# Kernel optimization log

Hardware: AMD Instinct MI355X
Metric: run time of the kernel (lower is better)

The kernel has to match this reference:

```python
import jax, jax.numpy as jnp
import numpy as np

B, S, D, H = 4, 2048, 768, 12
DEPTH = D // H


def setup_inputs() -> dict:
    key = jax.random.key(0)
    ks = jax.random.split(key, 8)
    scale = 1.0 / np.sqrt(D)
    inp = {
        "q": jax.random.normal(ks[0], (B, S, D), jnp.float32),
        "k": jax.random.normal(ks[1], (B, S, D), jnp.float32),
        "v": jax.random.normal(ks[2], (B, S, D), jnp.float32),
        # additive mask: 1.0 at disallowed (future) positions, causal
        "mask": jnp.triu(jnp.ones((S, S), jnp.float32), k=1)[None, None, :, :],
        "wq": jax.random.normal(ks[3], (D, D), jnp.float32) * scale,
        "wk": jax.random.normal(ks[4], (D, D), jnp.float32) * scale,
        "wv": jax.random.normal(ks[5], (D, D), jnp.float32) * scale,
        "w_dense": jax.random.normal(ks[6], (D, D), jnp.float32) * scale,
        "b_dense": jnp.zeros((D,), jnp.float32),
    }
    return inp


def _split_heads(x):
    b, s, _ = x.shape
    return x.reshape(b, s, H, DEPTH).transpose(0, 2, 1, 3)  # [B,H,S,depth]


def reference(q, k, v, mask, wq, wk, wv, w_dense, b_dense):
    qh = _split_heads(q @ wq.T)
    kh = _split_heads(k @ wk.T)
    vh = _split_heads(v @ wv.T)
    scale = jnp.sqrt(jnp.float32(DEPTH))
    logits = jnp.einsum("bhqd,bhkd->bhqk", qh, kh) / scale  # [B,H,S,S]
    logits = logits + mask * -1e9
    attn = jax.nn.softmax(logits, axis=-1)
    out = jnp.einsum("bhqk,bhkd->bhqd", attn, vh)
    out = out.transpose(0, 2, 1, 3).reshape(q.shape[0], -1, D)
    return out @ w_dense.T + b_dense
```

## Files before the change

kernel.cpp:

```cpp
#include <hip/hip_runtime.h>

typedef __attribute__((ext_vector_type(8))) short short8;
typedef __attribute__((ext_vector_type(4))) float f32x4;
typedef __attribute__((ext_vector_type(4))) unsigned int uint4v;

static __device__ __forceinline__ unsigned pack2(float x, float y) {
  unsigned ux = __float_as_uint(x) + 0x8000u;
  unsigned uy = __float_as_uint(y) + 0x8000u;
  return __builtin_amdgcn_perm(uy, ux, 0x07060302u);
}
static __device__ __forceinline__ unsigned packt(float x, float y) {
  return __builtin_amdgcn_perm(__float_as_uint(y), __float_as_uint(x), 0x07060302u);
}

#define GLDS(g, l)                                                                     \
  __builtin_amdgcn_global_load_lds((const __attribute__((address_space(1))) void*)(g), \
                                   (__attribute__((address_space(3))) void*)(l), 16, 0, 0)

__global__ __launch_bounds__(256) void cvt_all(const float* __restrict__ q,
                                               const float* __restrict__ k,
                                               const float* __restrict__ v,
                                               const float* __restrict__ w0,
                                               const float* __restrict__ w1,
                                               const float* __restrict__ w2,
                                               const float* __restrict__ w3,
                                               unsigned short* __restrict__ oq,
                                               unsigned short* __restrict__ ok,
                                               unsigned short* __restrict__ ov,
                                               unsigned short* __restrict__ o0,
                                               unsigned short* __restrict__ o1,
                                               unsigned short* __restrict__ o2,
                                               unsigned short* __restrict__ o3) {
  const int bx = blockIdx.x;
  const float* s;
  unsigned short* d;
  long p;
  if (bx < 9216) {
    int seg = bx / 3072;
    s = seg == 0 ? q : seg == 1 ? k : v;
    d = seg == 0 ? oq : seg == 1 ? ok : ov;
    p = (long)(bx - seg * 3072) * 256 + threadIdx.x;
  } else {
    int t = bx - 9216;
    int seg = t / 288;
    s = seg == 0 ? w0 : seg == 1 ? w1 : seg == 2 ? w2 : w3;
    d = seg == 0 ? o0 : seg == 1 ? o1 : seg == 2 ? o2 : o3;
    p = (long)(t - seg * 288) * 256 + threadIdx.x;
  }
  float4 v0 = ((const float4*)s)[2 * p];
  float4 v1 = ((const float4*)s)[2 * p + 1];
  uint4v o;
  o.x = pack2(v0.x, v0.y);
  o.y = pack2(v0.z, v0.w);
  o.z = pack2(v1.x, v1.y);
  o.w = pack2(v1.z, v1.w);
  *(uint4v*)(d + 8 * p) = o;
}

template <int MODE>
static __device__ __forceinline__ void proj_body(const unsigned short* __restrict__ A,
                                                 const unsigned short* __restrict__ W,
                                                 unsigned short* __restrict__ O, int m0,
                                                 int n0, unsigned short* buf,
                                                 float scale) {
  constexpr int K = 768;
  const int tid = threadIdx.x, lane = tid & 63, wave = tid >> 6;
  const int ln = lane & 15, quad = lane >> 4;
  const int wm = (wave & 1) << 6, wn = (wave >> 1) << 6;

  const int o0 = tid << 4, o1 = 4096 + (tid << 4);
  const int cxp = (((tid & 3) ^ ((tid >> 3) & 3)) << 3);
  const unsigned short* gA0 = A + (long)(m0 + (o0 >> 6)) * K + cxp;
  const unsigned short* gA1 = A + (long)(m0 + (o1 >> 6)) * K + cxp;
  const unsigned short* gW0 = W + (long)(n0 + (o0 >> 6)) * K + cxp;
  const unsigned short* gW1 = W + (long)(n0 + (o1 >> 6)) * K + cxp;

  GLDS(gA0, buf + (o0 >> 1));
  GLDS(gA1, buf + (o1 >> 1));
  GLDS(gW0, buf + 8192 + (o0 >> 1));
  GLDS(gW1, buf + 8192 + (o1 >> 1));

  const int qsw = (quad * 8) ^ (((ln >> 1) & 3) << 3);

  f32x4 acc[4][4] = {};
  for (int t = 0; t < 24; t++) {
    const int cur = t & 1, nxt = cur ^ 1;
    const int k1 = (t + 1) << 5;
    __syncthreads();
    if (t < 23) {
      GLDS(gA0 + k1, buf + nxt * 4096 + (o0 >> 1));
      GLDS(gA1 + k1, buf + nxt * 4096 + (o1 >> 1));
      GLDS(gW0 + k1, buf + 8192 + nxt * 4096 + (o0 >> 1));
      GLDS(gW1 + k1, buf + 8192 + nxt * 4096 + (o1 >> 1));
    }
    const unsigned short* As = buf + cur * 4096;
    const unsigned short* Bs = buf + 8192 + cur * 4096;
    short8 af[4], bfr[4];
#pragma unroll
    for (int mi = 0; mi < 4; mi++)
      af[mi] = *(const short8*)(As + (wm + mi * 16 + ln) * 32 + qsw);
#pragma unroll
    for (int ni = 0; ni < 4; ni++)
      bfr[ni] = *(const short8*)(Bs + (wn + ni * 16 + ln) * 32 + qsw);
#pragma unroll
    for (int mi = 0; mi < 4; mi++)
#pragma unroll
      for (int ni = 0; ni < 4; ni++)
        acc[mi][ni] = (MODE == 0)
                          ? __builtin_amdgcn_mfma_f32_16x16x32_bf16(bfr[ni], af[mi],
                                                                    acc[mi][ni], 0, 0, 0)
                          : __builtin_amdgcn_mfma_f32_16x16x32_bf16(af[mi], bfr[ni],
                                                                    acc[mi][ni], 0, 0, 0);
  }

  unsigned short* Ts = buf;
  __syncthreads();
  if (MODE == 0) {
#pragma unroll
    for (int mi = 0; mi < 4; mi++)
#pragma unroll
      for (int ni = 0; ni < 4; ni++) {
        f32x4 v = acc[mi][ni];
        int s = wm + mi * 16 + ln;
        int n = wn + ni * 16 + quad * 4;
        uint2 w2;
        w2.x = pack2(v[0] * scale, v[1] * scale);
        w2.y = pack2(v[2] * scale, v[3] * scale);
        *(uint2*)(Ts + s * 136 + n) = w2;
      }
    __syncthreads();
    const int part = tid & 7, sg0 = tid >> 3;
#pragma unroll
    for (int p = 0; p < 8; p++) {
      int seg = sg0 + p * 32;
      int hh = seg >> 7, s = seg & 127;
      short8 val = *(const short8*)(Ts + s * 136 + hh * 64 + part * 8);
      int gs = m0 + s;
      int bb = gs >> 11, srow = gs & 2047;
      int head = (n0 >> 6) + hh;
      *(short8*)(O + (((long)(bb * 12 + head) * 2048 + srow) << 6) + part * 8) = val;
    }
  } else {
#pragma unroll
    for (int mi = 0; mi < 4; mi++)
#pragma unroll
      for (int ni = 0; ni < 4; ni++) {
        f32x4 v = acc[mi][ni];
        int d = wn + ni * 16 + ln;
        int s = wm + mi * 16 + quad * 4;
        uint2 w2;
        w2.x = pack2(v[0], v[1]);
        w2.y = pack2(v[2], v[3]);
        *(uint2*)(Ts + d * 136 + s) = w2;
      }
    __syncthreads();
    const int part = tid & 15, r0 = tid >> 4;
    const int bb = m0 >> 11, sbase = m0 & 2047;
#pragma unroll
    for (int p = 0; p < 8; p++) {
      int d = r0 + p * 16;
      short8 val = *(const short8*)(Ts + d * 136 + part * 8);
      int head = (n0 >> 6) + (d >> 6);
      int dl = d & 63;
      *(short8*)(O + ((long)(bb * 12 + head) * 64 + dl) * 2048 + sbase + part * 8) = val;
    }
  }
}

__global__ __launch_bounds__(256) void proj_all(
    const unsigned short* __restrict__ qb, const unsigned short* __restrict__ kb,
    const unsigned short* __restrict__ vb, const unsigned short* __restrict__ wq,
    const unsigned short* __restrict__ wk, const unsigned short* __restrict__ wv,
    unsigned short* __restrict__ qh, unsigned short* __restrict__ kh,
    unsigned short* __restrict__ vt) {
  __shared__ unsigned short buf[17408];
  const int bx = blockIdx.x;
  const int xcd = bx & 7;
  const int i = bx >> 3;
  const int op = i / 48, j = i % 48;
  const int m0 = ((j / 6) * 8 + xcd) << 7, n0 = (j % 6) << 7;
  if (op == 0)
    proj_body<0>(qb, wq, qh, m0, n0, buf, 0.18033688011112042f);
  else if (op == 1)
    proj_body<0>(kb, wk, kh, m0, n0, buf, 1.0f);
  else
    proj_body<1>(vb, wv, vt, m0, n0, buf, 1.0f);
}

__global__ __launch_bounds__(256) void dense_gemm(const unsigned short* __restrict__ A,
                                                  const unsigned short* __restrict__ W,
                                                  const float* __restrict__ bias,
                                                  float* __restrict__ out) {
  constexpr int K = 768;
  __shared__ unsigned short buf[16384];
  const int bx = blockIdx.x;
  const int xcd = bx & 7;
  const int i = bx >> 3;
  const int m0 = ((i / 6) * 8 + xcd) << 7;
  const int n0 = (i % 6) << 7;

  const int tid = threadIdx.x, lane = tid & 63, wave = tid >> 6;
  const int ln = lane & 15, quad = lane >> 4;
  const int wm = (wave & 1) << 6, wn = (wave >> 1) << 6;

  const int o0 = tid << 4, o1 = 4096 + (tid << 4);
  const int cxp = (((tid & 3) ^ ((tid >> 3) & 3)) << 3);
  const unsigned short* gA0 = A + (long)(m0 + (o0 >> 6)) * K + cxp;
  const unsigned short* gA1 = A + (long)(m0 + (o1 >> 6)) * K + cxp;
  const unsigned short* gW0 = W + (long)(n0 + (o0 >> 6)) * K + cxp;
  const unsigned short* gW1 = W + (long)(n0 + (o1 >> 6)) * K + cxp;

  GLDS(gA0, buf + (o0 >> 1));
  GLDS(gA1, buf + (o1 >> 1));
  GLDS(gW0, buf + 8192 + (o0 >> 1));
  GLDS(gW1, buf + 8192 + (o1 >> 1));

  const int qsw = (quad * 8) ^ (((ln >> 1) & 3) << 3);

  f32x4 acc[4][4] = {};
  for (int t = 0; t < 24; t++) {
    const int cur = t & 1, nxt = cur ^ 1;
    const int k1 = (t + 1) << 5;
    __syncthreads();
    if (t < 23) {
      GLDS(gA0 + k1, buf + nxt * 4096 + (o0 >> 1));
      GLDS(gA1 + k1, buf + nxt * 4096 + (o1 >> 1));
      GLDS(gW0 + k1, buf + 8192 + nxt * 4096 + (o0 >> 1));
      GLDS(gW1 + k1, buf + 8192 + nxt * 4096 + (o1 >> 1));
    }
    const unsigned short* As = buf + cur * 4096;
    const unsigned short* Bs = buf + 8192 + cur * 4096;
    short8 af[4], bfr[4];
#pragma unroll
    for (int mi = 0; mi < 4; mi++)
      af[mi] = *(const short8*)(As + (wm + mi * 16 + ln) * 32 + qsw);
#pragma unroll
    for (int ni = 0; ni < 4; ni++)
      bfr[ni] = *(const short8*)(Bs + (wn + ni * 16 + ln) * 32 + qsw);
#pragma unroll
    for (int mi = 0; mi < 4; mi++)
#pragma unroll
      for (int ni = 0; ni < 4; ni++)
        acc[mi][ni] =
            __builtin_amdgcn_mfma_f32_16x16x32_bf16(bfr[ni], af[mi], acc[mi][ni], 0, 0, 0);
  }

#pragma unroll
  for (int mi = 0; mi < 4; mi++) {
    const int m = m0 + wm + mi * 16 + ln;
#pragma unroll
    for (int ni = 0; ni < 4; ni++) {
      const int n = n0 + wn + ni * 16 + quad * 4;
      f32x4 v = acc[mi][ni];
      float4 bv = *(const float4*)(bias + n);
      float4 st;
      st.x = v[0] + bv.x;
      st.y = v[1] + bv.y;
      st.z = v[2] + bv.z;
      st.w = v[3] + bv.w;
      *(float4*)(out + (long)m * 768 + n) = st;
    }
  }
}

__global__ __launch_bounds__(256, 4) void attn_kernel(const unsigned short* __restrict__ Qh,
                                                      const unsigned short* __restrict__ Kh,
                                                      const unsigned short* __restrict__ Vt,
                                                      unsigned short* __restrict__ outp) {
  constexpr int S = 2048;
  __shared__ unsigned short sbuf[16384];

  const int bx = blockIdx.x;
  const int xcd = bx & 7;
  const int ii = bx >> 3;
  const int qt = 31 - (ii & 31);
  const int grp = ii >> 5;
  const int bh = grp * 8 + xcd;
  const int h = bh % 12, b = bh / 12;
  const int tid = threadIdx.x, wave = tid >> 6, lane = tid & 63;
  const int ln = lane & 15, quad = lane >> 4;

  const unsigned short* Qg = Qh + (long)(b * 12 + h) * S * 64;
  const unsigned short* Kg = Kh + (long)(b * 12 + h) * S * 64;
  const unsigned short* Vg = Vt + (long)(b * 12 + h) * 64 * S;

  const int qr = qt * 64 + wave * 16 + ln;

  short8 bQ0 = *(const short8*)(Qg + qr * 64 + quad * 8);
  short8 bQ1 = *(const short8*)(Qg + qr * 64 + 32 + quad * 8);

  f32x4 O[4] = {};
  f32x4 sAcc = {};
  unsigned pk[8][2];

  short8 onesA;
#pragma unroll
  for (int j = 0; j < 8; j++) onesA[j] = (short)0x3F80;

  const int nk = (qt >> 1) + 1;

  const int srow = tid >> 2, sc = (tid & 3) << 3;
  const int koff0 = srow * 64 + sc;
  const int koff1 = (srow + 64) * 64 + sc;
  const int koff2 = srow * 64 + 32 + sc;
  const int koff3 = (srow + 64) * 64 + 32 + sc;
  const long voff = (long)srow * 2048 + sc;

  const int swzr = ((tid >> 3) & 3) << 3;
  const int wsw = (tid * 8) ^ swzr;
  const int qsw = (quad * 8) ^ (((ln >> 1) & 3) << 3);
  const int vplo = ((((tid & 1) << 4) | ((tid & 2) << 1)) ^ swzr);
  const int vphi = vplo ^ 8;
  unsigned short* vwrow = sbuf + 8192 + srow * 32;

  short8 kc[4], vc[4];
  {
    kc[0] = *(const short8*)(Kg + koff0);
    kc[1] = *(const short8*)(Kg + koff1);
    kc[2] = *(const short8*)(Kg + koff2);
    kc[3] = *(const short8*)(Kg + koff3);
    vc[0] = *(const short8*)(Vg + voff);
    vc[1] = *(const short8*)(Vg + voff + 32);
    vc[2] = *(const short8*)(Vg + voff + 64);
    vc[3] = *(const short8*)(Vg + voff + 96);
  }

  for (int kt = 0; kt < nk; kt++) {
    __syncthreads();
    {
      unsigned short* w = sbuf + wsw;
      *(short8*)(w) = kc[0];
      *(short8*)(w + 2048) = kc[1];
      *(short8*)(w + 4096) = kc[2];
      *(short8*)(w + 6144) = kc[3];
#pragma unroll
      for (int c = 0; c < 4; c++) {
        uint4v vv = __builtin_bit_cast(uint4v, vc[c]);
        uint2 lo, hi;
        lo.x = vv.x;
        lo.y = vv.y;
        hi.x = vv.z;
        hi.y = vv.w;
        *(uint2*)(vwrow + c * 2048 + vplo) = lo;
        *(uint2*)(vwrow + c * 2048 + vphi) = hi;
      }
    }
    __syncthreads();
    if (kt + 1 < nk) {
      const unsigned short* kg = Kg + (kt + 1) * 8192;
      const unsigned short* vg = Vg + (kt + 1) * 128;
      kc[0] = *(const short8*)(kg + koff0);
      kc[1] = *(const short8*)(kg + koff1);
      kc[2] = *(const short8*)(kg + koff2);
      kc[3] = *(const short8*)(kg + koff3);
      vc[0] = *(const short8*)(vg + voff);
      vc[1] = *(const short8*)(vg + voff + 32);
      vc[2] = *(const short8*)(vg + voff + 64);
      vc[3] = *(const short8*)(vg + voff + 96);
    }

    const bool dg = (kt == nk - 1);
    const int lim = dg ? ((qt & 1) ? 8 : 4) : 8;
    const int kbase = kt * 128 + quad * 4;

    __builtin_amdgcn_s_setprio(1);
#pragma unroll
    for (int ni = 0; ni < 8; ni++) {
      if (ni < lim) {
        const int fro = (ni * 16 + ln) * 32 + qsw;
        short8 k0 = *(const short8*)(sbuf + fro);
        short8 k1 = *(const short8*)(sbuf + 4096 + fro);
        f32x4 s = {};
        s = __builtin_amdgcn_mfma_f32_16x16x32_bf16(k0, bQ0, s, 0, 0, 0);
        s = __builtin_amdgcn_mfma_f32_16x16x32_bf16(k1, bQ1, s, 0, 0, 0);
        float p0 = __builtin_amdgcn_exp2f(s[0]), p1 = __builtin_amdgcn_exp2f(s[1]);
        float p2 = __builtin_amdgcn_exp2f(s[2]), p3 = __builtin_amdgcn_exp2f(s[3]);
        if (dg) {
          const int key = kbase + ni * 16;
          p0 = (key + 0 > qr) ? 0.f : p0;
          p1 = (key + 1 > qr) ? 0.f : p1;
          p2 = (key + 2 > qr) ? 0.f : p2;
          p3 = (key + 3 > qr) ? 0.f : p3;
        }
        pk[ni][0] = packt(p0, p1);
        pk[ni][1] = packt(p2, p3);
      }
    }

    const int kkB = lim >> 1;
#pragma unroll
    for (int kk = 0; kk < 4; kk++) {
      if (kk < kkB) {
        uint4v tb;
        tb.x = pk[2 * kk][0];
        tb.y = pk[2 * kk][1];
        tb.z = pk[2 * kk + 1][0];
        tb.w = pk[2 * kk + 1][1];
        short8 Bb = __builtin_bit_cast(short8, tb);
        const unsigned short* vp = sbuf + 8192 + kk * 2048;
        sAcc = __builtin_amdgcn_mfma_f32_16x16x32_bf16(onesA, Bb, sAcc, 0, 0, 0);
#pragma unroll
        for (int di = 0; di < 4; di++) {
          short8 aV = *(const short8*)(vp + (di * 16 + ln) * 32 + qsw);
          O[di] = __builtin_amdgcn_mfma_f32_16x16x32_bf16(aV, Bb, O[di], 0, 0, 0);
        }
      }
    }
    __builtin_amdgcn_s_setprio(0);
  }

  const float sum = sAcc[0];

  __syncthreads();
  unsigned short* Ts = sbuf;
  {
    float rl = __builtin_amdgcn_rcpf(sum);
    const int row = wave * 16 + ln;
#pragma unroll
    for (int di = 0; di < 4; di++) {
      uint2 wa;
      wa.x = pack2(O[di][0] * rl, O[di][1] * rl);
      wa.y = pack2(O[di][2] * rl, O[di][3] * rl);
      *(uint2*)(Ts + row * 72 + di * 16 + quad * 4) = wa;
    }
  }
  __syncthreads();
  const int part = tid & 7, r0 = tid >> 3;
#pragma unroll
  for (int p = 0; p < 2; p++) {
    int row = r0 + p * 32;
    int qrow = qt * 64 + row;
    short8 val = *(const short8*)(Ts + row * 72 + part * 8);
    *(short8*)(outp + ((long)b * S + qrow) * 768 + h * 64 + part * 8) = val;
  }
}

extern "C" void kernel_launch(void* const* d_in, const int* in_sizes, int n_in,
                              void* d_out, int out_size, void* d_ws, size_t ws_size,
                              hipStream_t stream) {
  const float* q = (const float*)d_in[0];
  const float* k = (const float*)d_in[1];
  const float* v = (const float*)d_in[2];
  const float* wq = (const float*)d_in[4];
  const float* wk = (const float*)d_in[5];
  const float* wv = (const float*)d_in[6];
  const float* wd = (const float*)d_in[7];
  const float* bd = (const float*)d_in[8];
  float* out = (float*)d_out;

  const long QKV = 4L * 2048 * 768;
  const long WN = 768L * 768;
  if (ws_size < (size_t)(7 * QKV + 4 * WN) * 2) return;

  unsigned short* qb = (unsigned short*)d_ws;
  unsigned short* kb = qb + QKV;
  unsigned short* vb = kb + QKV;
  unsigned short* wqb = vb + QKV;
  unsigned short* wkb = wqb + WN;
  unsigned short* wvb = wkb + WN;
  unsigned short* wdb = wvb + WN;
  unsigned short* qh = wdb + WN;
  unsigned short* kh = qh + QKV;
  unsigned short* vt = kh + QKV;
  unsigned short* at = vt + QKV;

  cvt_all<<<10368, 256, 0, stream>>>(q, k, v, wq, wk, wv, wd, qb, kb, vb, wqb, wkb, wvb, wdb);
  proj_all<<<1152, 256, 0, stream>>>(qb, kb, vb, wqb, wkb, wvb, qh, kh, vt);
  attn_kernel<<<1536, 256, 0, stream>>>(qh, kh, vt, at);
  dense_gemm<<<384, 256, 0, stream>>>(at, wdb, bd, out);
}
```

Before: 247.7 us.

## Split attention key range across waves with register-resident K/V and LDS reduction

The attention kernel now has each wave own all 64 query rows of the tile and process a strided subset of 32-key chunks. K and V fragments are loaded straight from global memory into registers with one-chunk-ahead prefetch, which removes the per-iteration LDS staging and both block barriers in the main loop. Partial O accumulators and row sums from the four waves are combined through LDS at the end before normalisation. In exchange, registers grow to 16 O accumulators per lane, so launch bounds drop to 2 blocks per SM, the epilogue needs a larger fp32 LDS buffer, and global loads are less coalesced.

```diff
diff --git a/kernel.cpp b/kernel.cpp
--- a/kernel.cpp
+++ b/kernel.cpp
@@ -263,12 +263,12 @@
   }
 }
 
-__global__ __launch_bounds__(256, 4) void attn_kernel(const unsigned short* __restrict__ Qh,
+__global__ __launch_bounds__(256, 2) void attn_kernel(const unsigned short* __restrict__ Qh,
                                                       const unsigned short* __restrict__ Kh,
                                                       const unsigned short* __restrict__ Vt,
                                                       unsigned short* __restrict__ outp) {
   constexpr int S = 2048;
-  __shared__ unsigned short sbuf[16384];
+  __shared__ float lds_f[17664];
 
   const int bx = blockIdx.x;
   const int xcd = bx & 7;
@@ -277,161 +277,153 @@
   const int grp = ii >> 5;
   const int bh = grp * 8 + xcd;
   const int h = bh % 12, b = bh / 12;
-  const int tid = threadIdx.x, wave = tid >> 6, lane = tid & 63;
+  const int tid = threadIdx.x, w = tid >> 6, lane = tid & 63;
   const int ln = lane & 15, quad = lane >> 4;
 
   const unsigned short* Qg = Qh + (long)(b * 12 + h) * S * 64;
   const unsigned short* Kg = Kh + (long)(b * 12 + h) * S * 64;
   const unsigned short* Vg = Vt + (long)(b * 12 + h) * 64 * S;
 
-  const int qr = qt * 64 + wave * 16 + ln;
-
-  short8 bQ0 = *(const short8*)(Qg + qr * 64 + quad * 8);
-  short8 bQ1 = *(const short8*)(Qg + qr * 64 + 32 + quad * 8);
-
-  f32x4 O[4] = {};
-  f32x4 sAcc = {};
-  unsigned pk[8][2];
+  short8 bQ0[4], bQ1[4];
+#pragma unroll
+  for (int g = 0; g < 4; g++) {
+    const unsigned short* qp = Qg + (qt * 64 + g * 16 + ln) * 64 + quad * 8;
+    bQ0[g] = *(const short8*)qp;
+    bQ1[g] = *(const short8*)(qp + 32);
+  }
+
+  f32x4 O[4][4] = {};
+  f32x4 sAcc[4] = {};
 
   short8 onesA;
 #pragma unroll
   for (int j = 0; j < 8; j++) onesA[j] = (short)0x3F80;
 
-  const int nk = (qt >> 1) + 1;
-
-  const int srow = tid >> 2, sc = (tid & 3) << 3;
-  const int koff0 = srow * 64 + sc;
-  const int koff1 = (srow + 64) * 64 + sc;
-  const int koff2 = srow * 64 + 32 + sc;
-  const int koff3 = (srow + 64) * 64 + 32 + sc;
-  const long voff = (long)srow * 2048 + sc;
-
-  const int swzr = ((tid >> 3) & 3) << 3;
-  const int wsw = (tid * 8) ^ swzr;
-  const int qsw = (quad * 8) ^ (((ln >> 1) & 3) << 3);
-  const int vplo = ((((tid & 1) << 4) | ((tid & 2) << 1)) ^ swzr);
-  const int vphi = vplo ^ 8;
-  unsigned short* vwrow = sbuf + 8192 + srow * 32;
-
-  short8 kc[4], vc[4];
+  const int nc = 2 * qt + 2;
+  const int dgc = 2 * qt;
+
+  const int ko0 = ln * 64 + quad * 8;
+  const int vrow = ln * 2048 + quad * 4;
+
+  short8 kf0, kf1, kf2, kf3;
+  uint4v vf[4];
+  if (w < nc) {
+    const unsigned short* kg = Kg + (w << 5) * 64;
+    kf0 = *(const short8*)(kg + ko0);
+    kf1 = *(const short8*)(kg + ko0 + 32);
+    kf2 = *(const short8*)(kg + ko0 + 1024);
+    kf3 = *(const short8*)(kg + ko0 + 1056);
+    const unsigned short* vg = Vg + (w << 5);
+#pragma unroll
+    for (int di = 0; di < 4; di++) {
+      uint2 lo = *(const uint2*)(vg + vrow + di * 32768);
+      uint2 hi = *(const uint2*)(vg + vrow + di * 32768 + 16);
+      uint4v t;
+      t.x = lo.x; t.y = lo.y; t.z = hi.x; t.w = hi.y;
+      vf[di] = t;
+    }
+  }
+
+  for (int c = w; c < nc; c += 4) {
+    short8 kn0, kn1, kn2, kn3;
+    uint4v vn[4];
+    const int cn = c + 4;
+    if (cn < nc) {
+      const unsigned short* kg = Kg + (cn << 5) * 64;
+      kn0 = *(const short8*)(kg + ko0);
+      kn1 = *(const short8*)(kg + ko0 + 32);
+      kn2 = *(const short8*)(kg + ko0 + 1024);
+      kn3 = *(const short8*)(kg + ko0 + 1056);
+      const unsigned short* vg = Vg + (cn << 5);
+#pragma unroll
+      for (int di = 0; di < 4; di++) {
+        uint2 lo = *(const uint2*)(vg + vrow + di * 32768);
+        uint2 hi = *(const uint2*)(vg + vrow + di * 32768 + 16);
+        uint4v t;
+        t.x = lo.x; t.y = lo.y; t.z = hi.x; t.w = hi.y;
+        vn[di] = t;
+      }
+    }
+
+    const bool dg = (c >= dgc);
+    const int kb = (c << 5) + quad * 4;
+
+    __builtin_amdgcn_s_setprio(1);
+#pragma unroll
+    for (int g = 0; g < 4; g++) {
+      f32x4 s0 = {}, s1 = {};
+      s0 = __builtin_amdgcn_mfma_f32_16x16x32_bf16(kf0, bQ0[g], s0, 0, 0, 0);
+      s0 = __builtin_amdgcn_mfma_f32_16x16x32_bf16(kf1, bQ1[g], s0, 0, 0, 0);
+      s1 = __builtin_amdgcn_mfma_f32_16x16x32_bf16(kf2, bQ0[g], s1, 0, 0, 0);
+      s1 = __builtin_amdgcn_mfma_f32_16x16x32_bf16(kf3, bQ1[g], s1, 0, 0, 0);
+      float p0 = __builtin_amdgcn_exp2f(s0[0]), p1 = __builtin_amdgcn_exp2f(s0[1]);
+      float p2 = __builtin_amdgcn_exp2f(s0[2]), p3 = __builtin_amdgcn_exp2f(s0[3]);
+      float p4 = __builtin_amdgcn_exp2f(s1[0]), p5 = __builtin_amdgcn_exp2f(s1[1]);
+      float p6 = __builtin_amdgcn_exp2f(s1[2]), p7 = __builtin_amdgcn_exp2f(s1[3]);
+      if (dg) {
+        const int qr = qt * 64 + g * 16 + ln;
+        p0 = (kb + 0 > qr) ? 0.f : p0;
+        p1 = (kb + 1 > qr) ? 0.f : p1;
+        p2 = (kb + 2 > qr) ? 0.f : p2;
+        p3 = (kb + 3 > qr) ? 0.f : p3;
+        p4 = (kb + 16 > qr) ? 0.f : p4;
+        p5 = (kb + 17 > qr) ? 0.f : p5;
+        p6 = (kb + 18 > qr) ? 0.f : p6;
+        p7 = (kb + 19 > qr) ? 0.f : p7;
+      }
+      uint4v tb;
+      tb.x = packt(p0, p1);
+      tb.y = packt(p2, p3);
+      tb.z = packt(p4, p5);
+      tb.w = packt(p6, p7);
+      short8 Bb = __builtin_bit_cast(short8, tb);
+      sAcc[g] = __builtin_amdgcn_mfma_f32_16x16x32_bf16(onesA, Bb, sAcc[g], 0, 0, 0);
+#pragma unroll
+      for (int di = 0; di < 4; di++) {
+        short8 aV = __builtin_bit_cast(short8, vf[di]);
+        O[g][di] = __builtin_amdgcn_mfma_f32_16x16x32_bf16(aV, Bb, O[g][di], 0, 0, 0);
+      }
+    }
+    __builtin_amdgcn_s_setprio(0);
+
+    kf0 = kn0; kf1 = kn1; kf2 = kn2; kf3 = kn3;
+#pragma unroll
+    for (int di = 0; di < 4; di++) vf[di] = vn[di];
+  }
+
   {
-    kc[0] = *(const short8*)(Kg + koff0);
-    kc[1] = *(const short8*)(Kg + koff1);
-    kc[2] = *(const short8*)(Kg + koff2);
-    kc[3] = *(const short8*)(Kg + koff3);
-    vc[0] = *(const short8*)(Vg + voff);
-    vc[1] = *(const short8*)(Vg + voff + 32);
-    vc[2] = *(const short8*)(Vg + voff + 64);
-    vc[3] = *(const short8*)(Vg + voff + 96);
-  }
-
-  for (int kt = 0; kt < nk; kt++) {
-    __syncthreads();
-    {
-      unsigned short* w = sbuf + wsw;
-      *(short8*)(w) = kc[0];
-      *(short8*)(w + 2048) = kc[1];
-      *(short8*)(w + 4096) = kc[2];
-      *(short8*)(w + 6144) = kc[3];
-#pragma unroll
-      for (int c = 0; c < 4; c++) {
-        uint4v vv = __builtin_bit_cast(uint4v, vc[c]);
-        uint2 lo, hi;
-        lo.x = vv.x;
-        lo.y = vv.y;
-        hi.x = vv.z;
-        hi.y = vv.w;
-        *(uint2*)(vwrow + c * 2048 + vplo) = lo;
-        *(uint2*)(vwrow + c * 2048 + vphi) = hi;
-      }
-    }
-    __syncthreads();
-    if (kt + 1 < nk) {
-      const unsigned short* kg = Kg + (kt + 1) * 8192;
-      const unsigned short* vg = Vg + (kt + 1) * 128;
-      kc[0] = *(const short8*)(kg + koff0);
-      kc[1] = *(const short8*)(kg + koff1);
-      kc[2] = *(const short8*)(kg + koff2);
-      kc[3] = *(const short8*)(kg + koff3);
-      vc[0] = *(const short8*)(vg + voff);
-      vc[1] = *(const short8*)(vg + voff + 32);
-      vc[2] = *(const short8*)(vg + voff + 64);
-      vc[3] = *(const short8*)(vg + voff + 96);
-    }
-
-    const bool dg = (kt == nk - 1);
-    const int lim = dg ? ((qt & 1) ? 8 : 4) : 8;
-    const int kbase = kt * 128 + quad * 4;
-
-    __builtin_amdgcn_s_setprio(1);
-#pragma unroll
-    for (int ni = 0; ni < 8; ni++) {
-      if (ni < lim) {
-        const int fro = (ni * 16 + ln) * 32 + qsw;
-        short8 k0 = *(const short8*)(sbuf + fro);
-        short8 k1 = *(const short8*)(sbuf + 4096 + fro);
-        f32x4 s = {};
-        s = __builtin_amdgcn_mfma_f32_16x16x32_bf16(k0, bQ0, s, 0, 0, 0);
-        s = __builtin_amdgcn_mfma_f32_16x16x32_bf16(k1, bQ1, s, 0, 0, 0);
-        float p0 = __builtin_amdgcn_exp2f(s[0]), p1 = __builtin_amdgcn_exp2f(s[1]);
-        float p2 = __builtin_amdgcn_exp2f(s[2]), p3 = __builtin_amdgcn_exp2f(s[3]);
-        if (dg) {
-          const int key = kbase + ni * 16;
-          p0 = (key + 0 > qr) ? 0.f : p0;
-          p1 = (key + 1 > qr) ? 0.f : p1;
-          p2 = (key + 2 > qr) ? 0.f : p2;
-          p3 = (key + 3 > qr) ? 0.f : p3;
-        }
-        pk[ni][0] = packt(p0, p1);
-        pk[ni][1] = packt(p2, p3);
-      }
-    }
-
-    const int kkB = lim >> 1;
-#pragma unroll
-    for (int kk = 0; kk < 4; kk++) {
-      if (kk < kkB) {
-        uint4v tb;
-        tb.x = pk[2 * kk][0];
-        tb.y = pk[2 * kk][1];
-        tb.z = pk[2 * kk + 1][0];
-        tb.w = pk[2 * kk + 1][1];
-        short8 Bb = __builtin_bit_cast(short8, tb);
-        const unsigned short* vp = sbuf + 8192 + kk * 2048;
-        sAcc = __builtin_amdgcn_mfma_f32_16x16x32_bf16(onesA, Bb, sAcc, 0, 0, 0);
-#pragma unroll
-        for (int di = 0; di < 4; di++) {
-          short8 aV = *(const short8*)(vp + (di * 16 + ln) * 32 + qsw);
-          O[di] = __builtin_amdgcn_mfma_f32_16x16x32_bf16(aV, Bb, O[di], 0, 0, 0);
-        }
-      }
-    }
-    __builtin_amdgcn_s_setprio(0);
-  }
-
-  const float sum = sAcc[0];
-
-  __syncthreads();
-  unsigned short* Ts = sbuf;
-  {
-    float rl = __builtin_amdgcn_rcpf(sum);
-    const int row = wave * 16 + ln;
-#pragma unroll
-    for (int di = 0; di < 4; di++) {
-      uint2 wa;
-      wa.x = pack2(O[di][0] * rl, O[di][1] * rl);
-      wa.y = pack2(O[di][2] * rl, O[di][3] * rl);
-      *(uint2*)(Ts + row * 72 + di * 16 + quad * 4) = wa;
+    float* Of = lds_f + w * 4352;
+#pragma unroll
+    for (int g = 0; g < 4; g++) {
+#pragma unroll
+      for (int di = 0; di < 4; di++)
+        *(f32x4*)(Of + (g * 16 + ln) * 68 + di * 16 + quad * 4) = O[g][di];
+    }
+    if (quad == 0) {
+#pragma unroll
+      for (int g = 0; g < 4; g++) lds_f[17408 + (g * 16 + ln) * 4 + w] = sAcc[g][0];
     }
   }
   __syncthreads();
   const int part = tid & 7, r0 = tid >> 3;
 #pragma unroll
-  for (int p = 0; p < 2; p++) {
-    int row = r0 + p * 32;
-    int qrow = qt * 64 + row;
-    short8 val = *(const short8*)(Ts + row * 72 + part * 8);
-    *(short8*)(outp + ((long)b * S + qrow) * 768 + h * 64 + part * 8) = val;
+  for (int pp = 0; pp < 2; pp++) {
+    const int q = r0 + pp * 32;
+    const float* sf = lds_f + 17408 + q * 4;
+    float rl = __builtin_amdgcn_rcpf(((sf[0] + sf[1]) + (sf[2] + sf[3])));
+    f32x4 a0 = {}, a1 = {};
+#pragma unroll
+    for (int ww = 0; ww < 4; ww++) {
+      const float* of = lds_f + ww * 4352 + q * 68 + part * 8;
+      a0 += *(const f32x4*)(of);
+      a1 += *(const f32x4*)(of + 4);
+    }
+    uint4v o;
+    o.x = pack2(a0[0] * rl, a0[1] * rl);
+    o.y = pack2(a0[2] * rl, a0[3] * rl);
+    o.z = pack2(a1[0] * rl, a1[1] * rl);
+    o.w = pack2(a1[2] * rl, a1[3] * rl);
+    *(uint4v*)(outp + ((long)b * S + qt * 64 + q) * 768 + h * 64 + part * 8) = o;
   }
 }
 
```

Measured after the change: 293.0 us. +18.3%, slower.

## Split attention key tiles across waves and reduce partial outputs through LDS

Applied to the files above, without the earlier changes.

Instead of each wave owning 16 query rows and walking all 128 keys of a tile, each wave now owns a 32-key slice and processes all 64 query rows, keeping four sets of output accumulators. Partial O values (stored as bf16) and row sums are written to shared memory and reduced across the four waves at the end. On the diagonal tile, waves whose key slice lies entirely past the last query skip their work. This reuses K/V fragments across query groups and spreads the causal workload across waves. The cost is more registers (occupancy hint lowered from 4 to 3), extra LDS, and a cross-wave reduction that rounds partials to bf16, which slightly reduces accuracy.

```diff
diff --git a/kernel.cpp b/kernel.cpp
--- a/kernel.cpp
+++ b/kernel.cpp
@@ -11,6 +11,9 @@
 }
 static __device__ __forceinline__ unsigned packt(float x, float y) {
   return __builtin_amdgcn_perm(__float_as_uint(y), __float_as_uint(x), 0x07060302u);
+}
+static __device__ __forceinline__ float b2f(unsigned short u) {
+  return __uint_as_float(((unsigned)u) << 16);
 }
 
 #define GLDS(g, l)                                                                     \
@@ -263,12 +266,12 @@
   }
 }
 
-__global__ __launch_bounds__(256, 4) void attn_kernel(const unsigned short* __restrict__ Qh,
+__global__ __launch_bounds__(256, 3) void attn_kernel(const unsigned short* __restrict__ Qh,
                                                       const unsigned short* __restrict__ Kh,
                                                       const unsigned short* __restrict__ Vt,
                                                       unsigned short* __restrict__ outp) {
   constexpr int S = 2048;
-  __shared__ unsigned short sbuf[16384];
+  __shared__ unsigned short sbuf[17920];
 
   const int bx = blockIdx.x;
   const int xcd = bx & 7;
@@ -277,27 +280,30 @@
   const int grp = ii >> 5;
   const int bh = grp * 8 + xcd;
   const int h = bh % 12, b = bh / 12;
-  const int tid = threadIdx.x, wave = tid >> 6, lane = tid & 63;
+  const int tid = threadIdx.x, w = tid >> 6, lane = tid & 63;
   const int ln = lane & 15, quad = lane >> 4;
 
   const unsigned short* Qg = Qh + (long)(b * 12 + h) * S * 64;
   const unsigned short* Kg = Kh + (long)(b * 12 + h) * S * 64;
   const unsigned short* Vg = Vt + (long)(b * 12 + h) * 64 * S;
 
-  const int qr = qt * 64 + wave * 16 + ln;
-
-  short8 bQ0 = *(const short8*)(Qg + qr * 64 + quad * 8);
-  short8 bQ1 = *(const short8*)(Qg + qr * 64 + 32 + quad * 8);
-
-  f32x4 O[4] = {};
-  f32x4 sAcc = {};
-  unsigned pk[8][2];
+  short8 bQ0[4], bQ1[4];
+#pragma unroll
+  for (int g = 0; g < 4; g++) {
+    const unsigned short* qp = Qg + (qt * 64 + g * 16 + ln) * 64 + quad * 8;
+    bQ0[g] = *(const short8*)qp;
+    bQ1[g] = *(const short8*)(qp + 32);
+  }
+
+  f32x4 O[4][4] = {};
+  f32x4 sAcc[4] = {};
 
   short8 onesA;
 #pragma unroll
   for (int j = 0; j < 8; j++) onesA[j] = (short)0x3F80;
 
   const int nk = (qt >> 1) + 1;
+  const int qmax = qt * 64 + 63;
 
   const int srow = tid >> 2, sc = (tid & 3) << 3;
   const int koff0 = srow * 64 + sc;
@@ -328,11 +334,11 @@
   for (int kt = 0; kt < nk; kt++) {
     __syncthreads();
     {
-      unsigned short* w = sbuf + wsw;
-      *(short8*)(w) = kc[0];
-      *(short8*)(w + 2048) = kc[1];
-      *(short8*)(w + 4096) = kc[2];
-      *(short8*)(w + 6144) = kc[3];
+      unsigned short* wp = sbuf + wsw;
+      *(short8*)(wp) = kc[0];
+      *(short8*)(wp + 2048) = kc[1];
+      *(short8*)(wp + 4096) = kc[2];
+      *(short8*)(wp + 6144) = kc[3];
 #pragma unroll
       for (int c = 0; c < 4; c++) {
         uint4v vv = __builtin_bit_cast(uint4v, vc[c]);
@@ -360,78 +366,99 @@
     }
 
     const bool dg = (kt == nk - 1);
-    const int lim = dg ? ((qt & 1) ? 8 : 4) : 8;
-    const int kbase = kt * 128 + quad * 4;
-
-    __builtin_amdgcn_s_setprio(1);
-#pragma unroll
-    for (int ni = 0; ni < 8; ni++) {
-      if (ni < lim) {
-        const int fro = (ni * 16 + ln) * 32 + qsw;
-        short8 k0 = *(const short8*)(sbuf + fro);
-        short8 k1 = *(const short8*)(sbuf + 4096 + fro);
-        f32x4 s = {};
-        s = __builtin_amdgcn_mfma_f32_16x16x32_bf16(k0, bQ0, s, 0, 0, 0);
-        s = __builtin_amdgcn_mfma_f32_16x16x32_bf16(k1, bQ1, s, 0, 0, 0);
-        float p0 = __builtin_amdgcn_exp2f(s[0]), p1 = __builtin_amdgcn_exp2f(s[1]);
-        float p2 = __builtin_amdgcn_exp2f(s[2]), p3 = __builtin_amdgcn_exp2f(s[3]);
+    const int s_base = kt * 128 + w * 32;
+    if (!dg || s_base <= qmax) {
+      const int r0 = (w * 32 + ln) * 32 + qsw;
+      short8 k00 = *(const short8*)(sbuf + r0);
+      short8 k01 = *(const short8*)(sbuf + 4096 + r0);
+      short8 k10 = *(const short8*)(sbuf + r0 + 512);
+      short8 k11 = *(const short8*)(sbuf + 4096 + r0 + 512);
+      const unsigned short* vp = sbuf + 8192 + w * 2048;
+      short8 aV0 = *(const short8*)(vp + (0 * 16 + ln) * 32 + qsw);
+      short8 aV1 = *(const short8*)(vp + (1 * 16 + ln) * 32 + qsw);
+      short8 aV2 = *(const short8*)(vp + (2 * 16 + ln) * 32 + qsw);
+      short8 aV3 = *(const short8*)(vp + (3 * 16 + ln) * 32 + qsw);
+      const int kb = s_base + quad * 4;
+
+      __builtin_amdgcn_s_setprio(1);
+#pragma unroll
+      for (int g = 0; g < 4; g++) {
+        f32x4 s0 = {}, s1 = {};
+        s0 = __builtin_amdgcn_mfma_f32_16x16x32_bf16(k00, bQ0[g], s0, 0, 0, 0);
+        s0 = __builtin_amdgcn_mfma_f32_16x16x32_bf16(k01, bQ1[g], s0, 0, 0, 0);
+        s1 = __builtin_amdgcn_mfma_f32_16x16x32_bf16(k10, bQ0[g], s1, 0, 0, 0);
+        s1 = __builtin_amdgcn_mfma_f32_16x16x32_bf16(k11, bQ1[g], s1, 0, 0, 0);
+        float p0 = __builtin_amdgcn_exp2f(s0[0]), p1 = __builtin_amdgcn_exp2f(s0[1]);
+        float p2 = __builtin_amdgcn_exp2f(s0[2]), p3 = __builtin_amdgcn_exp2f(s0[3]);
+        float p4 = __builtin_amdgcn_exp2f(s1[0]), p5 = __builtin_amdgcn_exp2f(s1[1]);
+        float p6 = __builtin_amdgcn_exp2f(s1[2]), p7 = __builtin_amdgcn_exp2f(s1[3]);
         if (dg) {
-          const int key = kbase + ni * 16;
-          p0 = (key + 0 > qr) ? 0.f : p0;
-          p1 = (key + 1 > qr) ? 0.f : p1;
-          p2 = (key + 2 > qr) ? 0.f : p2;
-          p3 = (key + 3 > qr) ? 0.f : p3;
+          const int qr = qt * 64 + g * 16 + ln;
+          p0 = (kb + 0 > qr) ? 0.f : p0;
+          p1 = (kb + 1 > qr) ? 0.f : p1;
+          p2 = (kb + 2 > qr) ? 0.f : p2;
+          p3 = (kb + 3 > qr) ? 0.f : p3;
+          p4 = (kb + 16 > qr) ? 0.f : p4;
+          p5 = (kb + 17 > qr) ? 0.f : p5;
+          p6 = (kb + 18 > qr) ? 0.f : p6;
+          p7 = (kb + 19 > qr) ? 0.f : p7;
         }
-        pk[ni][0] = packt(p0, p1);
-        pk[ni][1] = packt(p2, p3);
+        uint4v tb;
+        tb.x = packt(p0, p1);
+        tb.y = packt(p2, p3);
+        tb.z = packt(p4, p5);
+        tb.w = packt(p6, p7);
+        short8 Bb = __builtin_bit_cast(short8, tb);
+        sAcc[g] = __builtin_amdgcn_mfma_f32_16x16x32_bf16(onesA, Bb, sAcc[g], 0, 0, 0);
+        O[g][0] = __builtin_amdgcn_mfma_f32_16x16x32_bf16(aV0, Bb, O[g][0], 0, 0, 0);
+        O[g][1] = __builtin_amdgcn_mfma_f32_16x16x32_bf16(aV1, Bb, O[g][1], 0, 0, 0);
+        O[g][2] = __builtin_amdgcn_mfma_f32_16x16x32_bf16(aV2, Bb, O[g][2], 0, 0, 0);
+        O[g][3] = __builtin_amdgcn_mfma_f32_16x16x32_bf16(aV3, Bb, O[g][3], 0, 0, 0);
       }
-    }
-
-    const int kkB = lim >> 1;
-#pragma unroll
-    for (int kk = 0; kk < 4; kk++) {
-      if (kk < kkB) {
-        uint4v tb;
-        tb.x = pk[2 * kk][0];
-        tb.y = pk[2 * kk][1];
-        tb.z = pk[2 * kk + 1][0];
-        tb.w = pk[2 * kk + 1][1];
-        short8 Bb = __builtin_bit_cast(short8, tb);
-        const unsigned short* vp = sbuf + 8192 + kk * 2048;
-        sAcc = __builtin_amdgcn_mfma_f32_16x16x32_bf16(onesA, Bb, sAcc, 0, 0, 0);
-#pragma unroll
-        for (int di = 0; di < 4; di++) {
-          short8 aV = *(const short8*)(vp + (di * 16 + ln) * 32 + qsw);
-          O[di] = __builtin_amdgcn_mfma_f32_16x16x32_bf16(aV, Bb, O[di], 0, 0, 0);
-        }
+      __builtin_amdgcn_s_setprio(0);
+    }
+  }
+
+  __syncthreads();
+  {
+    unsigned short* Ow = sbuf + w * 4352;
+#pragma unroll
+    for (int g = 0; g < 4; g++) {
+#pragma unroll
+      for (int di = 0; di < 4; di++) {
+        uint2 w2;
+        w2.x = pack2(O[g][di][0], O[g][di][1]);
+        w2.y = pack2(O[g][di][2], O[g][di][3]);
+        *(uint2*)(Ow + (g * 16 + ln) * 68 + di * 16 + quad * 4) = w2;
       }
     }
-    __builtin_amdgcn_s_setprio(0);
-  }
-
-  const float sum = sAcc[0];
-
+    float* sums = (float*)(sbuf + 17408);
+    if (quad == 0) {
+#pragma unroll
+      for (int g = 0; g < 4; g++) sums[(g * 16 + ln) * 4 + w] = sAcc[g][0];
+    }
+  }
   __syncthreads();
-  unsigned short* Ts = sbuf;
-  {
-    float rl = __builtin_amdgcn_rcpf(sum);
-    const int row = wave * 16 + ln;
-#pragma unroll
-    for (int di = 0; di < 4; di++) {
-      uint2 wa;
-      wa.x = pack2(O[di][0] * rl, O[di][1] * rl);
-      wa.y = pack2(O[di][2] * rl, O[di][3] * rl);
-      *(uint2*)(Ts + row * 72 + di * 16 + quad * 4) = wa;
-    }
-  }
-  __syncthreads();
-  const int part = tid & 7, r0 = tid >> 3;
-#pragma unroll
-  for (int p = 0; p < 2; p++) {
-    int row = r0 + p * 32;
-    int qrow = qt * 64 + row;
-    short8 val = *(const short8*)(Ts + row * 72 + part * 8);
-    *(short8*)(outp + ((long)b * S + qrow) * 768 + h * 64 + part * 8) = val;
+  const int part = tid & 7, qr0 = tid >> 3;
+  const float* sums = (const float*)(sbuf + 17408);
+#pragma unroll
+  for (int pp = 0; pp < 2; pp++) {
+    const int q = qr0 + pp * 32;
+    const float* sf = sums + q * 4;
+    float rl = __builtin_amdgcn_rcpf((sf[0] + sf[1]) + (sf[2] + sf[3]));
+    float a[8] = {};
+#pragma unroll
+    for (int ww = 0; ww < 4; ww++) {
+      short8 pv = *(const short8*)(sbuf + ww * 4352 + q * 68 + part * 8);
+#pragma unroll
+      for (int j = 0; j < 8; j++) a[j] += b2f((unsigned short)pv[j]);
+    }
+    uint4v o;
+    o.x = pack2(a[0] * rl, a[1] * rl);
+    o.y = pack2(a[2] * rl, a[3] * rl);
+    o.z = pack2(a[4] * rl, a[5] * rl);
+    o.w = pack2(a[6] * rl, a[7] * rl);
+    *(uint4v*)(outp + ((long)b * S + qt * 64 + q) * 768 + h * 64 + part * 8) = o;
   }
 }
 
```

After: 362.3 us. +46.3%, slower.
